# Kernel tuning notes

Hardware: AMD Instinct MI355X
Metric: run time of the kernel (lower is better)

## Reference

```python
import jax, jax.numpy as jnp
import numpy as np

B, T, I = 8, 128, 196
TEXT_DIM, IMAGE_DIM, HIDDEN = 768, 1024, 512


def setup_inputs() -> dict:
    key = jax.random.key(0)
    ks = jax.random.split(key, 7)
    s = lambda d: 1.0 / np.sqrt(d)
    return {
        "text_features": jax.random.normal(ks[0], (B, T, TEXT_DIM), jnp.float32),
        "image_features": jax.random.normal(ks[1], (B, I, IMAGE_DIM), jnp.float32),
        "Wt": jax.random.normal(ks[2], (TEXT_DIM, HIDDEN), jnp.float32) * s(TEXT_DIM),
        "bt": jax.random.normal(ks[3], (HIDDEN,), jnp.float32) * s(TEXT_DIM),
        "Wi": jax.random.normal(ks[4], (IMAGE_DIM, HIDDEN), jnp.float32) * s(IMAGE_DIM),
        "bi": jax.random.normal(ks[5], (HIDDEN,), jnp.float32) * s(IMAGE_DIM),
        "wa": jax.random.normal(ks[6], (HIDDEN,), jnp.float32) * s(HIDDEN),
        "ba": jnp.zeros((1,), jnp.float32),
    }


def reference(text_features, image_features, Wt, bt, Wi, bi, wa, ba):
    # projections: [B,T,H] and [B,I,H]
    pt = jnp.einsum("btd,dh->bth", text_features, Wt) + bt
    pi = jnp.einsum("bid,dh->bih", image_features, Wi) + bi
    # additive Bahdanau scores: tanh of broadcast sum [B,T,I,H], reduced by wa
    h = jnp.tanh(pt[:, :, None, :] + pi[:, None, :, :])
    scores = jnp.einsum("btih,h->bti", h, wa) + ba[0]  # [B,T,I]
    text_attended = jnp.einsum("bti,bid->btd", jax.nn.softmax(scores, axis=-1), image_features)
    image_attended = jnp.einsum("bti,btd->bid", jax.nn.softmax(scores, axis=1), text_features)
    return text_attended, image_attended
```

## Files before the change

### kernel.cpp

```cpp
#include <hip/hip_runtime.h>
#include <math.h>

#define B 8
#define T 128
#define I_TOK 196
#define TEXT_DIM 768
#define IMAGE_DIM 1024
#define HIDDEN 512
#define EXP_SCALE 2.88539008177792681f

#if __has_builtin(__builtin_amdgcn_exp2f)
#define FAST_EXP2(x) __builtin_amdgcn_exp2f(x)
#else
#define FAST_EXP2(x) exp2f(x)
#endif
#if __has_builtin(__builtin_amdgcn_rcpf)
#define FAST_RCP(x) __builtin_amdgcn_rcpf(x)
#else
#define FAST_RCP(x) __fdividef(1.f, (x))
#endif
#if __has_builtin(__builtin_amdgcn_sched_barrier)
#define SCHED_FENCE() __builtin_amdgcn_sched_barrier(0)
#else
#define SCHED_FENCE()
#endif

typedef short bf16x8 __attribute__((ext_vector_type(8)));
typedef float f32x4 __attribute__((ext_vector_type(4)));

#define KT_T (TEXT_DIM / 32)
#define KT_I (IMAGE_DIM / 32)
#define MT_T (B * T / 16)
#define MT_I (B * I_TOK / 16)
#define NT   (HIDDEN / 16)

#define XT_ELEMS (MT_T * KT_T * 512)
#define XI_ELEMS (MT_I * KT_I * 512)
#define X_ELEMS  (XT_ELEMS + XI_ELEMS)
#define WT_T_ELEMS (NT * KT_T * 512)
#define W_ELEMS (WT_T_ELEMS + NT * KT_I * 512)

#define XTILES_T (MT_T * KT_T)
#define XTILES   (XTILES_T + MT_I * KT_I)
#define WTILES_T (NT * KT_T)
#define WTILES   (WTILES_T + NT * KT_I)
#define PREP_GRID ((XTILES + WTILES) / 4)

__device__ __forceinline__ unsigned short f2bf(float x) {
    unsigned int u = __float_as_uint(x);
    unsigned int r = u + 0x7FFFu + ((u >> 16) & 1u);
    return (unsigned short)(r >> 16);
}
__device__ __forceinline__ float bf2f(unsigned short h) {
    return __uint_as_float(((unsigned int)h) << 16);
}

__global__ __launch_bounds__(256) void prep_kernel(
        const float* __restrict__ text, const float* __restrict__ image,
        const float* __restrict__ Wt, const float* __restrict__ Wi,
        unsigned short* __restrict__ Xh, unsigned short* __restrict__ Xl,
        unsigned short* __restrict__ WTh, unsigned short* __restrict__ WTl)
{
    const int tid = threadIdx.x;
    const int lane = tid & 63, wv = tid >> 6;
    const int r16 = lane & 15, quad = lane >> 4;
    const int id = blockIdx.x * 4 + wv;

    float v[8];
    unsigned short* oh;
    unsigned short* ol;
    long dst;

    if (id < XTILES) {
        const float* X; int K, mt, kt;
        if (id < XTILES_T) { X = text; K = TEXT_DIM; mt = id / KT_T; kt = id % KT_T; }
        else { const int i2 = id - XTILES_T; X = image; K = IMAGE_DIM; mt = i2 / KT_I; kt = i2 % KT_I; }
        const float* src = X + (long)(mt * 16 + r16) * K + kt * 32 + quad * 8;
        const float4 a = *(const float4*)src;
        const float4 b = *(const float4*)(src + 4);
        v[0]=a.x; v[1]=a.y; v[2]=a.z; v[3]=a.w; v[4]=b.x; v[5]=b.y; v[6]=b.z; v[7]=b.w;
        oh = (id < XTILES_T) ? Xh : Xh + XT_ELEMS;
        ol = (id < XTILES_T) ? Xl : Xl + XT_ELEMS;
        const long tile = (id < XTILES_T) ? id : (long)(id - XTILES_T);
        dst = tile * 512 + lane * 8;
    } else {
        const int idw = id - XTILES;
        const float* W; int K, nt, kt;
        if (idw < WTILES_T) { W = Wt; K = TEXT_DIM; nt = idw / KT_T; kt = idw % KT_T; }
        else { const int i2 = idw - WTILES_T; W = Wi; K = IMAGE_DIM; nt = i2 / KT_I; kt = i2 % KT_I; }
        const float* src = W + (long)(kt * 32 + quad * 8) * HIDDEN + nt * 16 + r16;
        #pragma unroll
        for (int j = 0; j < 8; ++j) v[j] = src[(long)j * HIDDEN];
        oh = (idw < WTILES_T) ? WTh : WTh + WT_T_ELEMS;
        ol = (idw < WTILES_T) ? WTl : WTl + WT_T_ELEMS;
        const long tile = (idw < WTILES_T) ? idw : (long)(idw - WTILES_T);
        dst = tile * 512 + lane * 8;
    }

    uint4 hv, lv;
    unsigned int hh[8], ll[8];
    #pragma unroll
    for (int j = 0; j < 8; ++j) {
        hh[j] = f2bf(v[j]);
        ll[j] = f2bf(v[j] - bf2f((unsigned short)hh[j]));
    }
    hv.x = hh[0] | (hh[1] << 16); hv.y = hh[2] | (hh[3] << 16);
    hv.z = hh[4] | (hh[5] << 16); hv.w = hh[6] | (hh[7] << 16);
    lv.x = ll[0] | (ll[1] << 16); lv.y = ll[2] | (ll[3] << 16);
    lv.z = ll[4] | (ll[5] << 16); lv.w = ll[6] | (ll[7] << 16);
    *(uint4*)(oh + dst) = hv;
    *(uint4*)(ol + dst) = lv;
}

#define GT_BLOCKS (32 * 8)
#define GI_BLOCKS (49 * 8)
#define GEMM_GRID (GT_BLOCKS + GI_BLOCKS)
#define PSTRIDE 66

__global__ __launch_bounds__(256, 2) void mfma_proj_kernel(
        const unsigned short* __restrict__ Xh, const unsigned short* __restrict__ Xl,
        const unsigned short* __restrict__ WTh, const unsigned short* __restrict__ WTl,
        const float* __restrict__ bt, const float* __restrict__ bi,
        float* __restrict__ pt, float* __restrict__ pi)
{
    __shared__ float part[32 * PSTRIDE];

    const int tid = threadIdx.x;
    const int lane = tid & 63, wv = tid >> 6;
    const int r16 = lane & 15, quad = lane >> 4;
    const int nh = wv & 1;
    const int kh = wv >> 1;

    int bid = blockIdx.x;
    const unsigned short *xh, *xl, *wh, *wl; const float* bias; float* Y;
    int ktiles;
    if (bid < GT_BLOCKS) {
        xh = Xh; xl = Xl; wh = WTh; wl = WTl; bias = bt; Y = pt; ktiles = KT_T;
    } else {
        bid -= GT_BLOCKS;
        xh = Xh + XT_ELEMS; xl = Xl + XT_ELEMS;
        wh = WTh + WT_T_ELEMS; wl = WTl + WT_T_ELEMS;
        bias = bi; Y = pi; ktiles = KT_I;
    }
    const int m0 = (bid >> 3) * 32;
    const int n0 = (bid & 7) * 64 + nh * 32;
    const int nstep = ktiles >> 1;
    const int kt0 = kh * nstep;
    const int mt0 = (bid >> 3) * 2;
    const int nt0 = (bid & 7) * 4 + nh * 2;

    const unsigned short* pa0 = xh + ((long)mt0 * ktiles + kt0) * 512 + lane * 8;
    const unsigned short* pa1 = pa0 + (long)ktiles * 512;
    const unsigned short* qa0 = xl + ((long)mt0 * ktiles + kt0) * 512 + lane * 8;
    const unsigned short* qa1 = qa0 + (long)ktiles * 512;
    const unsigned short* pb0 = wh + ((long)nt0 * ktiles + kt0) * 512 + lane * 8;
    const unsigned short* pb1 = pb0 + (long)ktiles * 512;
    const unsigned short* qb0 = wl + ((long)nt0 * ktiles + kt0) * 512 + lane * 8;
    const unsigned short* qb1 = qb0 + (long)ktiles * 512;

    f32x4 a00 = {0,0,0,0}, a01 = {0,0,0,0}, a10 = {0,0,0,0}, a11 = {0,0,0,0};

    bf16x8 Ah0 = *(const bf16x8*)(pa0);
    bf16x8 Ah1 = *(const bf16x8*)(pa1);
    bf16x8 Al0 = *(const bf16x8*)(qa0);
    bf16x8 Al1 = *(const bf16x8*)(qa1);
    bf16x8 Bh0 = *(const bf16x8*)(pb0);
    bf16x8 Bh1 = *(const bf16x8*)(pb1);
    bf16x8 Bl0 = *(const bf16x8*)(qb0);
    bf16x8 Bl1 = *(const bf16x8*)(qb1);

    for (int s = 0; s < nstep; ++s) {
        const long kn = (s + 1 < nstep) ? (long)(s + 1) * 512 : 0;
        const bf16x8 nAh0 = *(const bf16x8*)(pa0 + kn);
        const bf16x8 nAh1 = *(const bf16x8*)(pa1 + kn);
        const bf16x8 nAl0 = *(const bf16x8*)(qa0 + kn);
        const bf16x8 nAl1 = *(const bf16x8*)(qa1 + kn);
        const bf16x8 nBh0 = *(const bf16x8*)(pb0 + kn);
        const bf16x8 nBh1 = *(const bf16x8*)(pb1 + kn);
        const bf16x8 nBl0 = *(const bf16x8*)(qb0 + kn);
        const bf16x8 nBl1 = *(const bf16x8*)(qb1 + kn);
        SCHED_FENCE();

        a00 = __builtin_amdgcn_mfma_f32_16x16x32_bf16(Ah0, Bh0, a00, 0, 0, 0);
        a01 = __builtin_amdgcn_mfma_f32_16x16x32_bf16(Ah0, Bh1, a01, 0, 0, 0);
        a10 = __builtin_amdgcn_mfma_f32_16x16x32_bf16(Ah1, Bh0, a10, 0, 0, 0);
        a11 = __builtin_amdgcn_mfma_f32_16x16x32_bf16(Ah1, Bh1, a11, 0, 0, 0);
        a00 = __builtin_amdgcn_mfma_f32_16x16x32_bf16(Ah0, Bl0, a00, 0, 0, 0);
        a01 = __builtin_amdgcn_mfma_f32_16x16x32_bf16(Ah0, Bl1, a01, 0, 0, 0);
        a10 = __builtin_amdgcn_mfma_f32_16x16x32_bf16(Ah1, Bl0, a10, 0, 0, 0);
        a11 = __builtin_amdgcn_mfma_f32_16x16x32_bf16(Ah1, Bl1, a11, 0, 0, 0);
        a00 = __builtin_amdgcn_mfma_f32_16x16x32_bf16(Al0, Bh0, a00, 0, 0, 0);
        a01 = __builtin_amdgcn_mfma_f32_16x16x32_bf16(Al0, Bh1, a01, 0, 0, 0);
        a10 = __builtin_amdgcn_mfma_f32_16x16x32_bf16(Al1, Bh0, a10, 0, 0, 0);
        a11 = __builtin_amdgcn_mfma_f32_16x16x32_bf16(Al1, Bh1, a11, 0, 0, 0);
        SCHED_FENCE();

        Ah0 = nAh0; Ah1 = nAh1; Al0 = nAl0; Al1 = nAl1;
        Bh0 = nBh0; Bh1 = nBh1; Bl0 = nBl0; Bl1 = nBl1;
    }

    const int lc = nh * 32 + r16;
    if (kh == 1) {
        #pragma unroll
        for (int r = 0; r < 4; ++r) {
            part[(quad * 4 + r) * PSTRIDE + lc]           = a00[r];
            part[(quad * 4 + r) * PSTRIDE + lc + 16]      = a01[r];
            part[(quad * 4 + 16 + r) * PSTRIDE + lc]      = a10[r];
            part[(quad * 4 + 16 + r) * PSTRIDE + lc + 16] = a11[r];
        }
    }
    __syncthreads();
    if (kh == 0) {
        const int row0 = m0 + quad * 4;
        const float bv0 = bias[n0 + r16];
        const float bv1 = bias[n0 + 16 + r16];
        #pragma unroll
        for (int r = 0; r < 4; ++r) {
            const float v00 = (a00[r] + part[(quad * 4 + r) * PSTRIDE + lc]           + bv0) * EXP_SCALE;
            const float v01 = (a01[r] + part[(quad * 4 + r) * PSTRIDE + lc + 16]      + bv1) * EXP_SCALE;
            const float v10 = (a10[r] + part[(quad * 4 + 16 + r) * PSTRIDE + lc]      + bv0) * EXP_SCALE;
            const float v11 = (a11[r] + part[(quad * 4 + 16 + r) * PSTRIDE + lc + 16] + bv1) * EXP_SCALE;
            Y[(long)(row0 + r)      * HIDDEN + n0 + r16]      = FAST_EXP2(v00);
            Y[(long)(row0 + r)      * HIDDEN + n0 + 16 + r16] = FAST_EXP2(v01);
            Y[(long)(row0 + 16 + r) * HIDDEN + n0 + r16]      = FAST_EXP2(v10);
            Y[(long)(row0 + 16 + r) * HIDDEN + n0 + 16 + r16] = FAST_EXP2(v11);
        }
    }
}

__global__ __launch_bounds__(256, 8) void scores_kernel(const float* __restrict__ pt,
        const float* __restrict__ pi, const float* __restrict__ wa,
        const float* __restrict__ ba, float* __restrict__ scores)
{
    const int blk = blockIdx.x;
    const int bt = blk >> 1;
    const int half = blk & 1;
    const int b = bt >> 7;
    const int tid = threadIdx.x;
    const int lane = tid & 63, wave = tid >> 6;

    const float* ptrow = pt + (long)bt * HIDDEN + lane * 8;
    const float4 pA = *(const float4*)ptrow;
    const float4 pB = *(const float4*)(ptrow + 4);
    float4 wA = *(const float4*)(wa + lane * 8);
    float4 wB = *(const float4*)(wa + lane * 8 + 4);

    float S = wA.x + wA.y + wA.z + wA.w + wB.x + wB.y + wB.z + wB.w;
    #pragma unroll
    for (int off = 32; off; off >>= 1) S += __shfl_down(S, off);
    const float base = S + ba[0];

    wA.x *= -2.f; wA.y *= -2.f; wA.z *= -2.f; wA.w *= -2.f;
    wB.x *= -2.f; wB.y *= -2.f; wB.z *= -2.f; wB.w *= -2.f;

    const float* pib = pi + (long)b * I_TOK * HIDDEN + lane * 8;
    const int i0 = half * 98 + wave;
    const int iend = half * 98 + 98;

    float4 ca = *(const float4*)(pib + (long)i0 * HIDDEN);
    float4 cb = *(const float4*)(pib + (long)i0 * HIDDEN + 4);

    for (int i = i0; i < iend; i += 4) {
        const int inx = (i + 4 < iend) ? (i + 4) : i;
        const float4 na = *(const float4*)(pib + (long)inx * HIDDEN);
        const float4 nb = *(const float4*)(pib + (long)inx * HIDDEN + 4);

        float acc = 0.f;
        acc = fmaf(wA.x, FAST_RCP(fmaf(pA.x, ca.x, 1.f)), acc);
        acc = fmaf(wA.y, FAST_RCP(fmaf(pA.y, ca.y, 1.f)), acc);
        acc = fmaf(wA.z, FAST_RCP(fmaf(pA.z, ca.z, 1.f)), acc);
        acc = fmaf(wA.w, FAST_RCP(fmaf(pA.w, ca.w, 1.f)), acc);
        acc = fmaf(wB.x, FAST_RCP(fmaf(pB.x, cb.x, 1.f)), acc);
        acc = fmaf(wB.y, FAST_RCP(fmaf(pB.y, cb.y, 1.f)), acc);
        acc = fmaf(wB.z, FAST_RCP(fmaf(pB.z, cb.z, 1.f)), acc);
        acc = fmaf(wB.w, FAST_RCP(fmaf(pB.w, cb.w, 1.f)), acc);

        #pragma unroll
        for (int off = 32; off; off >>= 1) acc += __shfl_down(acc, off);
        if (lane == 0) scores[(long)bt * I_TOK + i] = base + acc;
        ca = na; cb = nb;
    }
}

#define ATT_TEXT_BLOCKS (B * (T / 4) * 4)
#define ATT_IMG_BLOCKS  (3 * B * (I_TOK / 4))
#define ATT_GRID (ATT_TEXT_BLOCKS + ATT_IMG_BLOCKS)

__global__ __launch_bounds__(256) void att_kernel(const float* __restrict__ scores,
        const float* __restrict__ image, const float* __restrict__ text,
        float* __restrict__ out_text, float* __restrict__ out_img)
{
    __shared__ float sm[I_TOK * 4];
    const int tid = threadIdx.x, lane = tid & 63, wave = tid >> 6;

    if (blockIdx.x < ATT_TEXT_BLOCKS) {
        const int bid = blockIdx.x;
        const int csplit = bid & 3;
        const int grp = bid >> 2;
        const int b = grp >> 5;
        const int t0 = (grp & 31) * 4;

        {
            const float* srow = scores + ((long)(b * T + t0 + wave)) * I_TOK;
            const float s0 = srow[lane];
            const float s1 = srow[lane + 64];
            const float s2 = srow[lane + 128];
            const float s3 = (lane < 4) ? srow[lane + 192] : -INFINITY;
            float m = fmaxf(fmaxf(s0, s1), fmaxf(s2, s3));
            #pragma unroll
            for (int off = 32; off; off >>= 1) m = fmaxf(m, __shfl_xor(m, off));
            const float e0 = __expf(s0 - m);
            const float e1 = __expf(s1 - m);
            const float e2 = __expf(s2 - m);
            const float e3 = (lane < 4) ? __expf(s3 - m) : 0.f;
            float sum = e0 + e1 + e2 + e3;
            #pragma unroll
            for (int off = 32; off; off >>= 1) sum += __shfl_xor(sum, off);
            const float inv = __fdividef(1.0f, sum);
            sm[lane * 4 + wave] = e0 * inv;
            sm[(lane + 64) * 4 + wave] = e1 * inv;
            sm[(lane + 128) * 4 + wave] = e2 * inv;
            if (lane < 4) sm[(lane + 192) * 4 + wave] = e3 * inv;
        }
        __syncthreads();

        const float* img = image + (long)b * I_TOK * IMAGE_DIM + csplit * 256 + tid;
        float a0 = 0.f, a1 = 0.f, a2 = 0.f, a3 = 0.f;

        for (int g = 0; g < 49; ++g) {
            const int i = g * 4;
            const float v0 = img[(long)(i + 0) * IMAGE_DIM];
            const float v1 = img[(long)(i + 1) * IMAGE_DIM];
            const float v2 = img[(long)(i + 2) * IMAGE_DIM];
            const float v3 = img[(long)(i + 3) * IMAGE_DIM];
            const float4 p0 = *(const float4*)&sm[(i + 0) * 4];
            const float4 p1 = *(const float4*)&sm[(i + 1) * 4];
            const float4 p2 = *(const float4*)&sm[(i + 2) * 4];
            const float4 p3 = *(const float4*)&sm[(i + 3) * 4];
            a0 = fmaf(p0.x, v0, a0); a1 = fmaf(p0.y, v0, a1);
            a2 = fmaf(p0.z, v0, a2); a3 = fmaf(p0.w, v0, a3);
            a0 = fmaf(p1.x, v1, a0); a1 = fmaf(p1.y, v1, a1);
            a2 = fmaf(p1.z, v1, a2); a3 = fmaf(p1.w, v1, a3);
            a0 = fmaf(p2.x, v2, a0); a1 = fmaf(p2.y, v2, a1);
            a2 = fmaf(p2.z, v2, a2); a3 = fmaf(p2.w, v2, a3);
            a0 = fmaf(p3.x, v3, a0); a1 = fmaf(p3.y, v3, a1);
            a2 = fmaf(p3.z, v3, a2); a3 = fmaf(p3.w, v3, a3);
        }
        float* o = out_text + ((long)(b * T + t0)) * IMAGE_DIM + csplit * 256 + tid;
        o[0 * IMAGE_DIM] = a0;
        o[1 * IMAGE_DIM] = a1;
        o[2 * IMAGE_DIM] = a2;
        o[3 * IMAGE_DIM] = a3;
    } else {
        const int bid = blockIdx.x - ATT_TEXT_BLOCKS;
        const int csplit = bid / (B * (I_TOK / 4));
        const int g2 = bid % (B * (I_TOK / 4));
        const int b = g2 / (I_TOK / 4);
        const int i0 = (g2 % (I_TOK / 4)) * 4;

        {
            const float* sc = scores + (long)b * T * I_TOK + (i0 + wave);
            const float s0 = sc[(long)lane * I_TOK];
            const float s1 = sc[(long)(lane + 64) * I_TOK];
            float m = fmaxf(s0, s1);
            #pragma unroll
            for (int off = 32; off; off >>= 1) m = fmaxf(m, __shfl_xor(m, off));
            const float e0 = __expf(s0 - m);
            const float e1 = __expf(s1 - m);
            float sum = e0 + e1;
            #pragma unroll
            for (int off = 32; off; off >>= 1) sum += __shfl_xor(sum, off);
            const float inv = __fdividef(1.0f, sum);
            sm[lane * 4 + wave] = e0 * inv;
            sm[(lane + 64) * 4 + wave] = e1 * inv;
        }
        __syncthreads();

        const float* txt = text + (long)b * T * TEXT_DIM + csplit * 256 + tid;
        float a0 = 0.f, a1 = 0.f, a2 = 0.f, a3 = 0.f;

        for (int g = 0; g < 32; ++g) {
            const int t = g * 4;
            const float v0 = txt[(long)(t + 0) * TEXT_DIM];
            const float v1 = txt[(long)(t + 1) * TEXT_DIM];
            const float v2 = txt[(long)(t + 2) * TEXT_DIM];
            const float v3 = txt[(long)(t + 3) * TEXT_DIM];
            const float4 q0 = *(const float4*)&sm[(t + 0) * 4];
            const float4 q1 = *(const float4*)&sm[(t + 1) * 4];
            const float4 q2 = *(const float4*)&sm[(t + 2) * 4];
            const float4 q3 = *(const float4*)&sm[(t + 3) * 4];
            a0 = fmaf(q0.x, v0, a0); a1 = fmaf(q0.y, v0, a1);
            a2 = fmaf(q0.z, v0, a2); a3 = fmaf(q0.w, v0, a3);
            a0 = fmaf(q1.x, v1, a0); a1 = fmaf(q1.y, v1, a1);
            a2 = fmaf(q1.z, v1, a2); a3 = fmaf(q1.w, v1, a3);
            a0 = fmaf(q2.x, v2, a0); a1 = fmaf(q2.y, v2, a1);
            a2 = fmaf(q2.z, v2, a2); a3 = fmaf(q2.w, v2, a3);
            a0 = fmaf(q3.x, v3, a0); a1 = fmaf(q3.y, v3, a1);
            a2 = fmaf(q3.z, v3, a2); a3 = fmaf(q3.w, v3, a3);
        }
        float* o = out_img + ((long)b * I_TOK + i0) * TEXT_DIM + csplit * 256 + tid;
        o[0 * TEXT_DIM] = a0;
        o[1 * TEXT_DIM] = a1;
        o[2 * TEXT_DIM] = a2;
        o[3 * TEXT_DIM] = a3;
    }
}

extern "C" void kernel_launch(void* const* d_in, const int* in_sizes, int n_in,
                              void* d_out, int out_size, void* d_ws, size_t ws_size,
                              hipStream_t stream) {
    const float* text  = (const float*)d_in[0];
    const float* image = (const float*)d_in[1];
    const float* Wt    = (const float*)d_in[2];
    const float* bt    = (const float*)d_in[3];
    const float* Wi    = (const float*)d_in[4];
    const float* bi    = (const float*)d_in[5];
    const float* wa    = (const float*)d_in[6];
    const float* ba    = (const float*)d_in[7];

    float* pt = (float*)d_ws;
    float* pi = pt + (long)B * T * HIDDEN;
    float* sc = pi + (long)B * I_TOK * HIDDEN;
    unsigned short* Xh  = (unsigned short*)(sc + (long)B * T * I_TOK);
    unsigned short* Xl  = Xh + X_ELEMS;
    unsigned short* WTh = Xl + X_ELEMS;
    unsigned short* WTl = WTh + W_ELEMS;

    float* out_text = (float*)d_out;
    float* out_img  = out_text + (long)B * T * IMAGE_DIM;

    prep_kernel<<<PREP_GRID, 256, 0, stream>>>(text, image, Wt, Wi, Xh, Xl, WTh, WTl);
    mfma_proj_kernel<<<GEMM_GRID, 256, 0, stream>>>(Xh, Xl, WTh, WTl, bt, bi, pt, pi);
    scores_kernel<<<2 * B * T, 256, 0, stream>>>(pt, pi, wa, ba, sc);
    att_kernel<<<ATT_GRID, 256, 0, stream>>>(sc, image, text, out_text, out_img);
}
```

Measured before the change: 145.0 us.

## Register-block multiple rows per thread in scores and attention kernels

The scores kernel now handles four text rows per block, so each loaded image-projection row is reused across four accumulators and the grid shrinks fourfold. The attention kernel processes 8 text rows per block for the text side and 14 image tokens per block for the image side, so each global load of image or text features feeds more FMAs. The aim is fewer redundant global reads of pi, image and text. The cost is more registers per thread and fewer blocks, which may reduce occupancy and parallelism.

```diff
diff --git a/kernel.cpp b/kernel.cpp
--- a/kernel.cpp
+++ b/kernel.cpp
@@ -228,20 +228,25 @@
     }
 }
 
-__global__ __launch_bounds__(256, 8) void scores_kernel(const float* __restrict__ pt,
+__global__ __launch_bounds__(256) void scores_kernel(const float* __restrict__ pt,
         const float* __restrict__ pi, const float* __restrict__ wa,
         const float* __restrict__ ba, float* __restrict__ scores)
 {
     const int blk = blockIdx.x;
-    const int bt = blk >> 1;
-    const int half = blk & 1;
-    const int b = bt >> 7;
+    const int b = blk >> 6;
+    const int rem = blk & 63;
+    const int t0 = (rem >> 1) * 4;
+    const int half = rem & 1;
     const int tid = threadIdx.x;
     const int lane = tid & 63, wave = tid >> 6;
 
-    const float* ptrow = pt + (long)bt * HIDDEN + lane * 8;
-    const float4 pA = *(const float4*)ptrow;
-    const float4 pB = *(const float4*)(ptrow + 4);
+    float4 pA[4], pB[4];
+    #pragma unroll
+    for (int t = 0; t < 4; ++t) {
+        const float* ptrow = pt + (long)(b * T + t0 + t) * HIDDEN + lane * 8;
+        pA[t] = *(const float4*)ptrow;
+        pB[t] = *(const float4*)(ptrow + 4);
+    }
     float4 wA = *(const float4*)(wa + lane * 8);
     float4 wB = *(const float4*)(wa + lane * 8 + 4);
 
@@ -265,43 +270,54 @@
         const float4 na = *(const float4*)(pib + (long)inx * HIDDEN);
         const float4 nb = *(const float4*)(pib + (long)inx * HIDDEN + 4);
 
-        float acc = 0.f;
-        acc = fmaf(wA.x, FAST_RCP(fmaf(pA.x, ca.x, 1.f)), acc);
-        acc = fmaf(wA.y, FAST_RCP(fmaf(pA.y, ca.y, 1.f)), acc);
-        acc = fmaf(wA.z, FAST_RCP(fmaf(pA.z, ca.z, 1.f)), acc);
-        acc = fmaf(wA.w, FAST_RCP(fmaf(pA.w, ca.w, 1.f)), acc);
-        acc = fmaf(wB.x, FAST_RCP(fmaf(pB.x, cb.x, 1.f)), acc);
-        acc = fmaf(wB.y, FAST_RCP(fmaf(pB.y, cb.y, 1.f)), acc);
-        acc = fmaf(wB.z, FAST_RCP(fmaf(pB.z, cb.z, 1.f)), acc);
-        acc = fmaf(wB.w, FAST_RCP(fmaf(pB.w, cb.w, 1.f)), acc);
-
-        #pragma unroll
-        for (int off = 32; off; off >>= 1) acc += __shfl_down(acc, off);
-        if (lane == 0) scores[(long)bt * I_TOK + i] = base + acc;
+        float acc[4] = {0.f, 0.f, 0.f, 0.f};
+        #pragma unroll
+        for (int t = 0; t < 4; ++t) {
+            acc[t] = fmaf(wA.x, FAST_RCP(fmaf(pA[t].x, ca.x, 1.f)), acc[t]);
+            acc[t] = fmaf(wA.y, FAST_RCP(fmaf(pA[t].y, ca.y, 1.f)), acc[t]);
+            acc[t] = fmaf(wA.z, FAST_RCP(fmaf(pA[t].z, ca.z, 1.f)), acc[t]);
+            acc[t] = fmaf(wA.w, FAST_RCP(fmaf(pA[t].w, ca.w, 1.f)), acc[t]);
+            acc[t] = fmaf(wB.x, FAST_RCP(fmaf(pB[t].x, cb.x, 1.f)), acc[t]);
+            acc[t] = fmaf(wB.y, FAST_RCP(fmaf(pB[t].y, cb.y, 1.f)), acc[t]);
+            acc[t] = fmaf(wB.z, FAST_RCP(fmaf(pB[t].z, cb.z, 1.f)), acc[t]);
+            acc[t] = fmaf(wB.w, FAST_RCP(fmaf(pB[t].w, cb.w, 1.f)), acc[t]);
+        }
+        #pragma unroll
+        for (int t = 0; t < 4; ++t) {
+            #pragma unroll
+            for (int off = 32; off; off >>= 1) acc[t] += __shfl_down(acc[t], off);
+        }
+        if (lane == 0) {
+            #pragma unroll
+            for (int t = 0; t < 4; ++t)
+                scores[(long)(b * T + t0 + t) * I_TOK + i] = base + acc[t];
+        }
         ca = na; cb = nb;
     }
 }
 
-#define ATT_TEXT_BLOCKS (B * (T / 4) * 4)
-#define ATT_IMG_BLOCKS  (3 * B * (I_TOK / 4))
+#define ATT_TEXT_BLOCKS (B * (T / 8) * 4)
+#define ATT_IMG_BLOCKS  (3 * B * (I_TOK / 14))
 #define ATT_GRID (ATT_TEXT_BLOCKS + ATT_IMG_BLOCKS)
 
 __global__ __launch_bounds__(256) void att_kernel(const float* __restrict__ scores,
         const float* __restrict__ image, const float* __restrict__ text,
         float* __restrict__ out_text, float* __restrict__ out_img)
 {
-    __shared__ float sm[I_TOK * 4];
+    __shared__ float sm[2048];
     const int tid = threadIdx.x, lane = tid & 63, wave = tid >> 6;
 
     if (blockIdx.x < ATT_TEXT_BLOCKS) {
         const int bid = blockIdx.x;
         const int csplit = bid & 3;
         const int grp = bid >> 2;
-        const int b = grp >> 5;
-        const int t0 = (grp & 31) * 4;
-
-        {
-            const float* srow = scores + ((long)(b * T + t0 + wave)) * I_TOK;
+        const int b = grp >> 4;
+        const int t0 = (grp & 15) * 8;
+
+        #pragma unroll
+        for (int rr = 0; rr < 2; ++rr) {
+            const int r = wave + rr * 4;
+            const float* srow = scores + ((long)(b * T + t0 + r)) * I_TOK;
             const float s0 = srow[lane];
             const float s1 = srow[lane + 64];
             const float s2 = srow[lane + 128];
@@ -317,15 +333,15 @@
             #pragma unroll
             for (int off = 32; off; off >>= 1) sum += __shfl_xor(sum, off);
             const float inv = __fdividef(1.0f, sum);
-            sm[lane * 4 + wave] = e0 * inv;
-            sm[(lane + 64) * 4 + wave] = e1 * inv;
-            sm[(lane + 128) * 4 + wave] = e2 * inv;
-            if (lane < 4) sm[(lane + 192) * 4 + wave] = e3 * inv;
+            sm[lane * 8 + r] = e0 * inv;
+            sm[(lane + 64) * 8 + r] = e1 * inv;
+            sm[(lane + 128) * 8 + r] = e2 * inv;
+            if (lane < 4) sm[(lane + 192) * 8 + r] = e3 * inv;
         }
         __syncthreads();
 
         const float* img = image + (long)b * I_TOK * IMAGE_DIM + csplit * 256 + tid;
-        float a0 = 0.f, a1 = 0.f, a2 = 0.f, a3 = 0.f;
+        float acc[8] = {0.f,0.f,0.f,0.f,0.f,0.f,0.f,0.f};
 
         for (int g = 0; g < 49; ++g) {
             const int i = g * 4;
@@ -333,33 +349,30 @@
             const float v1 = img[(long)(i + 1) * IMAGE_DIM];
             const float v2 = img[(long)(i + 2) * IMAGE_DIM];
             const float v3 = img[(long)(i + 3) * IMAGE_DIM];
-            const float4 p0 = *(const float4*)&sm[(i + 0) * 4];
-            const float4 p1 = *(const float4*)&sm[(i + 1) * 4];
-            const float4 p2 = *(const float4*)&sm[(i + 2) * 4];
-            const float4 p3 = *(const float4*)&sm[(i + 3) * 4];
-            a0 = fmaf(p0.x, v0, a0); a1 = fmaf(p0.y, v0, a1);
-            a2 = fmaf(p0.z, v0, a2); a3 = fmaf(p0.w, v0, a3);
-            a0 = fmaf(p1.x, v1, a0); a1 = fmaf(p1.y, v1, a1);
-            a2 = fmaf(p1.z, v1, a2); a3 = fmaf(p1.w, v1, a3);
-            a0 = fmaf(p2.x, v2, a0); a1 = fmaf(p2.y, v2, a1);
-            a2 = fmaf(p2.z, v2, a2); a3 = fmaf(p2.w, v2, a3);
-            a0 = fmaf(p3.x, v3, a0); a1 = fmaf(p3.y, v3, a1);
-            a2 = fmaf(p3.z, v3, a2); a3 = fmaf(p3.w, v3, a3);
+            #pragma unroll
+            for (int k = 0; k < 4; ++k) {
+                const float vk = (k == 0) ? v0 : (k == 1) ? v1 : (k == 2) ? v2 : v3;
+                const float4 pa = *(const float4*)&sm[(i + k) * 8];
+                const float4 pb = *(const float4*)&sm[(i + k) * 8 + 4];
+                acc[0] = fmaf(pa.x, vk, acc[0]); acc[1] = fmaf(pa.y, vk, acc[1]);
+                acc[2] = fmaf(pa.z, vk, acc[2]); acc[3] = fmaf(pa.w, vk, acc[3]);
+                acc[4] = fmaf(pb.x, vk, acc[4]); acc[5] = fmaf(pb.y, vk, acc[5]);
+                acc[6] = fmaf(pb.z, vk, acc[6]); acc[7] = fmaf(pb.w, vk, acc[7]);
+            }
         }
         float* o = out_text + ((long)(b * T + t0)) * IMAGE_DIM + csplit * 256 + tid;
-        o[0 * IMAGE_DIM] = a0;
-        o[1 * IMAGE_DIM] = a1;
-        o[2 * IMAGE_DIM] = a2;
-        o[3 * IMAGE_DIM] = a3;
+        #pragma unroll
+        for (int r = 0; r < 8; ++r)
+            o[(long)r * IMAGE_DIM] = acc[r];
     } else {
         const int bid = blockIdx.x - ATT_TEXT_BLOCKS;
-        const int csplit = bid / (B * (I_TOK / 4));
-        const int g2 = bid % (B * (I_TOK / 4));
-        const int b = g2 / (I_TOK / 4);
-        const int i0 = (g2 % (I_TOK / 4)) * 4;
-
-        {
-            const float* sc = scores + (long)b * T * I_TOK + (i0 + wave);
+        const int csplit = bid / 112;
+        const int rem = bid % 112;
+        const int b = rem / 14;
+        const int i0 = (rem % 14) * 14;
+
+        for (int c = wave; c < 14; c += 4) {
+            const float* sc = scores + (long)b * T * I_TOK + (i0 + c);
             const float s0 = sc[(long)lane * I_TOK];
             const float s1 = sc[(long)(lane + 64) * I_TOK];
             float m = fmaxf(s0, s1);
@@ -371,13 +384,15 @@
             #pragma unroll
             for (int off = 32; off; off >>= 1) sum += __shfl_xor(sum, off);
             const float inv = __fdividef(1.0f, sum);
-            sm[lane * 4 + wave] = e0 * inv;
-            sm[(lane + 64) * 4 + wave] = e1 * inv;
+            sm[lane * 16 + c] = e0 * inv;
+            sm[(lane + 64) * 16 + c] = e1 * inv;
         }
         __syncthreads();
 
         const float* txt = text + (long)b * T * TEXT_DIM + csplit * 256 + tid;
-        float a0 = 0.f, a1 = 0.f, a2 = 0.f, a3 = 0.f;
+        float acc[14];
+        #pragma unroll
+        for (int r = 0; r < 14; ++r) acc[r] = 0.f;
 
         for (int g = 0; g < 32; ++g) {
             const int t = g * 4;
@@ -385,24 +400,26 @@
             const float v1 = txt[(long)(t + 1) * TEXT_DIM];
             const float v2 = txt[(long)(t + 2) * TEXT_DIM];
             const float v3 = txt[(long)(t + 3) * TEXT_DIM];
-            const float4 q0 = *(const float4*)&sm[(t + 0) * 4];
-            const float4 q1 = *(const float4*)&sm[(t + 1) * 4];
-            const float4 q2 = *(const float4*)&sm[(t + 2) * 4];
-            const float4 q3 = *(const float4*)&sm[(t + 3) * 4];
-            a0 = fmaf(q0.x, v0, a0); a1 = fmaf(q0.y, v0, a1);
-            a2 = fmaf(q0.z, v0, a2); a3 = fmaf(q0.w, v0, a3);
-            a0 = fmaf(q1.x, v1, a0); a1 = fmaf(q1.y, v1, a1);
-            a2 = fmaf(q1.z, v1, a2); a3 = fmaf(q1.w, v1, a3);
-            a0 = fmaf(q2.x, v2, a0); a1 = fmaf(q2.y, v2, a1);
-            a2 = fmaf(q2.z, v2, a2); a3 = fmaf(q2.w, v2, a3);
-            a0 = fmaf(q3.x, v3, a0); a1 = fmaf(q3.y, v3, a1);
-            a2 = fmaf(q3.z, v3, a2); a3 = fmaf(q3.w, v3, a3);
+            #pragma unroll
+            for (int k = 0; k < 4; ++k) {
+                const float vk = (k == 0) ? v0 : (k == 1) ? v1 : (k == 2) ? v2 : v3;
+                const float4 q0 = *(const float4*)&sm[(t + k) * 16];
+                const float4 q1 = *(const float4*)&sm[(t + k) * 16 + 4];
+                const float4 q2 = *(const float4*)&sm[(t + k) * 16 + 8];
+                const float2 q3 = *(const float2*)&sm[(t + k) * 16 + 12];
+                acc[0]  = fmaf(q0.x, vk, acc[0]);  acc[1]  = fmaf(q0.y, vk, acc[1]);
+                acc[2]  = fmaf(q0.z, vk, acc[2]);  acc[3]  = fmaf(q0.w, vk, acc[3]);
+                acc[4]  = fmaf(q1.x, vk, acc[4]);  acc[5]  = fmaf(q1.y, vk, acc[5]);
+                acc[6]  = fmaf(q1.z, vk, acc[6]);  acc[7]  = fmaf(q1.w, vk, acc[7]);
+                acc[8]  = fmaf(q2.x, vk, acc[8]);  acc[9]  = fmaf(q2.y, vk, acc[9]);
+                acc[10] = fmaf(q2.z, vk, acc[10]); acc[11] = fmaf(q2.w, vk, acc[11]);
+                acc[12] = fmaf(q3.x, vk, acc[12]); acc[13] = fmaf(q3.y, vk, acc[13]);
+            }
         }
         float* o = out_img + ((long)b * I_TOK + i0) * TEXT_DIM + csplit * 256 + tid;
-        o[0 * TEXT_DIM] = a0;
-        o[1 * TEXT_DIM] = a1;
-        o[2 * TEXT_DIM] = a2;
-        o[3 * TEXT_DIM] = a3;
+        #pragma unroll
+        for (int r = 0; r < 14; ++r)
+            o[(long)r * TEXT_DIM] = acc[r];
     }
 }
 
@@ -431,6 +448,6 @@
 
     prep_kernel<<<PREP_GRID, 256, 0, stream>>>(text, image, Wt, Wi, Xh, Xl, WTh, WTl);
     mfma_proj_kernel<<<GEMM_GRID, 256, 0, stream>>>(Xh, Xl, WTh, WTl, bt, bi, pt, pi);
-    scores_kernel<<<2 * B * T, 256, 0, stream>>>(pt, pi, wa, ba, sc);
+    scores_kernel<<<B * (T / 4) * 2, 256, 0, stream>>>(pt, pi, wa, ba, sc);
     att_kernel<<<ATT_GRID, 256, 0, stream>>>(sc, image, text, out_text, out_img);
 }
```

Measured after the change: 146.0 us. Within noise of the previous version (+0.7%).
